# Performance work log

Hardware: AMD Instinct MI355X
Metric: run time of the kernel (lower is better)

The kernel has to match this reference:

```python
import jax, jax.numpy as jnp
import numpy as np

B, TZ, TU = 32, 16, 128
E, H, V = 512, 1024, 32000
FREQ_THRES = 4   # cfg.freq_thres: zero out copy prob for most-frequent tokens
LN_EPS = 1e-3


def setup_inputs() -> dict:
    key = jax.random.key(0)
    ks = jax.random.split(key, 16)
    s = lambda k, shape, sc=0.02: jax.random.normal(k, shape, jnp.float32) * sc
    return dict(
        z_enc_out=jax.random.normal(ks[0], (TZ, B, H), jnp.float32),
        pz_proba=jax.nn.softmax(jax.random.normal(ks[1], (TZ, B, V), jnp.float32), axis=-1),
        u_enc_out=jax.random.normal(ks[2], (TU, B, H), jnp.float32),
        m_t_input=jax.random.randint(ks[3], (1, B), 0, V),
        last_hidden=jax.random.normal(ks[4], (1, B, H), jnp.float32),
        emb=s(ks[5], (V, E), 1.0 / np.sqrt(E)),
        Wa_z=s(ks[6], (2 * H, H)), ba_z=jnp.zeros((H,), jnp.float32), v_z=s(ks[7], (H,), 1.0 / np.sqrt(H)),
        Wa_u=s(ks[8], (2 * H, H)), ba_u=jnp.zeros((H,), jnp.float32), v_u=s(ks[9], (H,), 1.0 / np.sqrt(H)),
        W_ih=s(ks[10], (3 * H, E + 2 * H)), W_hh=s(ks[11], (3 * H, H)),
        b_ih=jnp.zeros((3 * H,), jnp.float32), b_hh=jnp.zeros((3 * H,), jnp.float32),
        ln_a=jnp.ones((H,), jnp.float32), ln_b=jnp.zeros((H,), jnp.float32),
        W_proj=s(ks[12], (H, V)), b_proj=jnp.zeros((V,), jnp.float32),
        W_c=s(ks[13], (2 * H, H)), b_c=jnp.zeros((H,), jnp.float32),
        W_v1=s(ks[14], (H, 1)), b_v1=jnp.zeros((1,), jnp.float32),
    )


def _attn(hidden, enc, Wa, ba, v):
    # hidden [1,B,H], enc [T,B,H] -> context [1,B,H]
    hh = jnp.broadcast_to(hidden, enc.shape)                       # [T,B,H]
    energy = jnp.tanh(jnp.concatenate([hh, enc], -1) @ Wa + ba)    # [T,B,H]
    scores = jnp.einsum('tbh,h->bt', energy, v)                    # [B,T]
    w = jax.nn.softmax(scores, axis=1)
    return jnp.einsum('bt,tbh->bh', w, enc)[None]                  # [1,B,H]


def _layernorm(x, a, b):
    mu = jnp.mean(x, axis=-1, keepdims=True)
    sigma = jnp.std(x, axis=-1, keepdims=True, ddof=1)  # torch.std is unbiased
    return (x - mu) / (sigma + LN_EPS) * a + b


def reference(z_enc_out, pz_proba, u_enc_out, m_t_input, last_hidden,
              emb, Wa_z, ba_z, v_z, Wa_u, ba_u, v_u,
              W_ih, W_hh, b_ih, b_hh, ln_a, ln_b,
              W_proj, b_proj, W_c, b_c, W_v1, b_v1):
    m_embed = emb[m_t_input]                                       # [1,B,E]
    z_ctx = _attn(last_hidden, z_enc_out, Wa_z, ba_z, v_z)         # [1,B,H]
    u_ctx = _attn(last_hidden, u_enc_out, Wa_u, ba_u, v_u)         # [1,B,H]
    x = jnp.concatenate([z_ctx, u_ctx, m_embed], -1)[0]            # [B,2H+E]
    h = last_hidden[0]                                             # [B,H]
    # single-step GRU (torch gate order: r, z, n)
    gi = x @ W_ih.T + b_ih
    gh = h @ W_hh.T + b_hh
    ir, iz, inn = jnp.split(gi, 3, axis=-1)
    hr, hz, hn = jnp.split(gh, 3, axis=-1)
    r = jax.nn.sigmoid(ir + hr)
    zg = jax.nn.sigmoid(iz + hz)
    n = jnp.tanh(inn + r * hn)
    h_new = (1.0 - zg) * n + zg * h                                # [B,H]
    gru_out = _layernorm(h_new, ln_a, ln_b)                        # [B,H]
    gen_score = gru_out @ W_proj + b_proj                          # [B,V]
    # tanh-linear copy score over z positions
    g_rep = jnp.broadcast_to(gru_out[None], z_enc_out.shape)       # [Tz,B,H]
    zc = jnp.tanh(jnp.concatenate([z_enc_out, g_rep], -1) @ W_c + b_c)  # [Tz,B,H]
    zc = (zc @ W_v1 + b_v1)[..., 0].T                              # [B,Tz]
    # joint softmax over [gen | copy]
    scores = jax.nn.softmax(jnp.concatenate([gen_score, zc], axis=1), axis=1)
    gen_p, copy_p = scores[:, :V], scores[:, V:]
    copy_v = jnp.einsum('bt,tbv->bv', copy_p, pz_proba)            # mask_prob bmm
    freq_mask = (jnp.arange(V) >= FREQ_THRES).astype(gen_p.dtype)
    proba = gen_p + copy_v * freq_mask
    return proba, h_new[None]
```

## Files before the change

### kernel.cpp

```cpp
#include <hip/hip_runtime.h>
#include <stdint.h>

#define B_ 32
#define TZ_ 16
#define TU_ 128
#define E_ 512
#define H_ 1024
#define V_ 32000
#define X_ 2560
#define H3_ 3072
#define LN_EPS_ 0.001f

#define NP_IH 20
#define NP_HH 16

typedef unsigned short ushort_t;
typedef ushort_t us4 __attribute__((ext_vector_type(4)));
typedef ushort_t us8 __attribute__((ext_vector_type(8)));
typedef short bf16x8 __attribute__((ext_vector_type(8)));
typedef float f32x4 __attribute__((ext_vector_type(4)));

__device__ __forceinline__ float bf2f(ushort_t u){
  union { unsigned int i; float f; } x; x.i = ((unsigned int)u) << 16; return x.f;
}
__device__ __forceinline__ ushort_t f2b(float f){
  union { float f; unsigned int i; } u; u.f = f;
  unsigned int x = u.i;
  return (ushort_t)((x + 0x7fffu + ((x >> 16) & 1u)) >> 16);
}
__device__ __forceinline__ bool is_bf(const void* lnA){
  return *(const unsigned int*)lnA == 0x3F803F80u;
}
__device__ __forceinline__ float ldg_(const void* p, size_t i, bool isb){
  return isb ? bf2f(((const ushort_t*)p)[i]) : ((const float*)p)[i];
}
__device__ __forceinline__ float sigm(float x){ return 1.0f/(1.0f + __expf(-x)); }
__device__ __forceinline__ float tanh_f(float x){
  float cx = fminf(fmaxf(x, -9.0f), 9.0f);
  float t = __expf(2.0f*cx);
  return (t - 1.0f)/(t + 1.0f);
}

__global__ void k0_init(const void* lh, const void* emb, const int* mt,
                        const void* ba_z, const void* ba_u, const void* b_c, const void* bpj,
                        const void* lnA,
                        float* h_f32, ushort_t* hb, float* x, float* hWaZ, float* hWaU,
                        float* sz, float* su, float* gruWc, float* genscore){
  bool isb = is_bf(lnA);
  int i = blockIdx.x*256 + threadIdx.x;
  if (i < 32768){ float v = ldg_(lh, i, isb); h_f32[i] = v; hb[i] = f2b(v); return; }
  i -= 32768;
  if (i < 16384){ int b = i >> 9, e = i & 511;
    x[b*X_ + 2048 + e] = ldg_(emb, (size_t)(unsigned)mt[b]*E_ + e, isb); return; }
  i -= 16384;
  if (i < 32768){ hWaZ[i] = ldg_(ba_z, i & 1023, isb); return; }
  i -= 32768;
  if (i < 32768){ hWaU[i] = ldg_(ba_u, i & 1023, isb); return; }
  i -= 32768;
  if (i < 4608){ if (i < 512) sz[i] = 0.f; else su[i-512] = 0.f; return; }
  i -= 4608;
  if (i < 32768){ gruWc[i] = ldg_(b_c, i & 1023, isb); return; }
  i -= 32768;
  if (i < 1024000){
    int b = i / V_;
    int v = i - b*V_;
    genscore[(size_t)b*V_ + v] = ldg_(bpj, v, isb);
    return;
  }
}

__global__ void kC_cvt(const void* uenc, const void* zenc, const void* Wih, const void* Whh,
                       const void* lnA,
                       ushort_t* uB, ushort_t* zB, ushort_t* WihB, ushort_t* WhhB){
  bool isb = is_bf(lnA);
  long long i = (long long)(blockIdx.x*256 + threadIdx.x) * 8;
  const long long NU = (long long)TU_*B_*H_;
  const long long NZ = (long long)TZ_*B_*H_;
  const long long NI = (long long)H3_*X_;
  const long long NH = (long long)H3_*H_;
  const void* src; ushort_t* dst;
  if (i < NU){ src = uenc; dst = uB; }
  else if ((i -= NU) < NZ){ src = zenc; dst = zB; }
  else if ((i -= NZ) < NI){ src = Wih; dst = WihB; }
  else if ((i -= NI) < NH){ src = Whh; dst = WhhB; }
  else return;
  if (isb){
    *(us8*)&dst[i] = *(const us8*)((const ushort_t*)src + i);
  } else {
    const float* s = (const float*)src + i;
    float4 a0 = *(const float4*)s, a1 = *(const float4*)(s + 4);
    us8 o;
    o[0]=f2b(a0.x); o[1]=f2b(a0.y); o[2]=f2b(a0.z); o[3]=f2b(a0.w);
    o[4]=f2b(a1.x); o[5]=f2b(a1.y); o[6]=f2b(a1.z); o[7]=f2b(a1.w);
    *(us8*)&dst[i] = o;
  }
}

__global__ void kX_cvt(const float* x, ushort_t* xb){
  int i = (blockIdx.x*256 + threadIdx.x) * 8;
  const float* s = x + i;
  float4 a0 = *(const float4*)s, a1 = *(const float4*)(s + 4);
  us8 o;
  o[0]=f2b(a0.x); o[1]=f2b(a0.y); o[2]=f2b(a0.z); o[3]=f2b(a0.w);
  o[4]=f2b(a1.x); o[5]=f2b(a1.y); o[6]=f2b(a1.z); o[7]=f2b(a1.w);
  *(us8*)&xb[i] = o;
}

__global__ void kT_transpose(const void* Wz, const void* Wu, const void* Wc, const void* lnA,
                             ushort_t* tZ, ushort_t* tU, ushort_t* tC,
                             ushort_t* tZt, ushort_t* tUt, ushort_t* tCb){
  bool isb = is_bf(lnA);
  int w = blockIdx.z;
  const void* src = (w==0||w==3)? Wz : (w==1||w==4)? Wu : Wc;
  size_t base = (w==0||w==1||w==5) ? (size_t)H_*H_ : 0;
  ushort_t* dst = (w==0)? tZ : (w==1)? tU : (w==2)? tC : (w==3)? tZt : (w==4)? tUt : tCb;
  __shared__ ushort_t T[64][68];
  int k0 = blockIdx.x*64, j0 = blockIdx.y*64;
  int tx = threadIdx.x & 15, ty = threadIdx.x >> 4;
  if (isb){
    const ushort_t* s = (const ushort_t*)src + base;
    #pragma unroll
    for (int rr=0; rr<4; ++rr){
      int row = ty + rr*16;
      *(us4*)&T[row][tx*4] = *(const us4*)&s[(size_t)(k0+row)*H_ + j0 + tx*4];
    }
  } else {
    const float* s = (const float*)src + base;
    #pragma unroll
    for (int rr=0; rr<4; ++rr){
      int row = ty + rr*16;
      #pragma unroll
      for (int c=0;c<4;c++)
        T[row][tx*4+c] = f2b(s[(size_t)(k0+row)*H_ + j0 + tx*4 + c]);
    }
  }
  __syncthreads();
  #pragma unroll
  for (int rr=0; rr<4; ++rr){
    int row = ty + rr*16;
    us4 o;
    o[0]=T[tx*4+0][row]; o[1]=T[tx*4+1][row]; o[2]=T[tx*4+2][row]; o[3]=T[tx*4+3][row];
    *(us4*)&dst[(size_t)(j0+row)*H_ + k0 + tx*4] = o;
  }
}

__global__ void kP_t(const void* Wp, const void* lnA, ushort_t* WpT){
  bool isb = is_bf(lnA);
  __shared__ ushort_t T[64][68];
  int h0 = blockIdx.x*64, v0 = blockIdx.y*64;
  int tx = threadIdx.x & 15, ty = threadIdx.x >> 4;
  if (isb){
    const ushort_t* s = (const ushort_t*)Wp;
    #pragma unroll
    for (int rr=0; rr<4; ++rr){
      int row = ty + rr*16;
      *(us4*)&T[row][tx*4] = *(const us4*)&s[(size_t)(h0+row)*V_ + v0 + tx*4];
    }
  } else {
    const float* s = (const float*)Wp;
    #pragma unroll
    for (int rr=0; rr<4; ++rr){
      int row = ty + rr*16;
      #pragma unroll
      for (int c=0;c<4;c++)
        T[row][tx*4+c] = f2b(s[(size_t)(h0+row)*V_ + v0 + tx*4 + c]);
    }
  }
  __syncthreads();
  #pragma unroll
  for (int rr=0; rr<4; ++rr){
    int row = ty + rr*16;
    us4 o;
    o[0]=T[tx*4+0][row]; o[1]=T[tx*4+1][row]; o[2]=T[tx*4+2][row]; o[3]=T[tx*4+3][row];
    *(us4*)&WpT[(size_t)(v0+row)*H_ + h0 + tx*4] = o;
  }
}

__global__ __launch_bounds__(256) void kg_mfma(const ushort_t* Ab0, const ushort_t* Ab1,
                                               const ushort_t* W0, const ushort_t* W1,
                                               float* out0, float* out1, int N){
  const ushort_t* Ab = blockIdx.z ? Ab1 : Ab0;
  const ushort_t* WT = blockIdx.z ? W1 : W0;
  float* out = blockIdx.z ? out1 : out0;
  int j0 = blockIdx.x*128;
  int kchunk = H_ / gridDim.y;
  int kb = blockIdx.y*kchunk;
  __shared__ ushort_t Bs[128*32];
  int tid = threadIdx.x, wid = tid >> 6, lane = tid & 63;
  int q = lane >> 4, n = lane & 15;
  int rrow = tid >> 2, t4 = tid & 3;
  f32x4 acc[2][2];
  #pragma unroll
  for (int r=0;r<2;r++)
    #pragma unroll
    for (int c=0;c<2;c++)
      #pragma unroll
      for (int e=0;e<4;e++) acc[r][c][e] = 0.f;

  for (int kt = 0; kt < kchunk; kt += 32){
    int k = kb + kt;
    __syncthreads();
    #pragma unroll
    for (int p=0;p<2;p++){
      const ushort_t* srcB = WT + (size_t)(j0 + p*64 + rrow)*H_ + k + t4*8;
      __builtin_amdgcn_global_load_lds(srcB, &Bs[(p*64 + wid*16)*32], 16, 0, 0);
    }
    __syncthreads();
    bf16x8 af[2], bfr[2];
    #pragma unroll
    for (int r=0;r<2;r++) af[r] = *(const bf16x8*)&Ab[(size_t)(r*16 + n)*H_ + k + q*8];
    #pragma unroll
    for (int c=0;c<2;c++) bfr[c] = *(const bf16x8*)&Bs[(wid*32 + c*16 + n)*32 + q*8];
    #pragma unroll
    for (int r=0;r<2;r++)
      #pragma unroll
      for (int c=0;c<2;c++)
        acc[r][c] = __builtin_amdgcn_mfma_f32_16x16x32_bf16(af[r], bfr[c], acc[r][c], 0, 0, 0);
  }
  #pragma unroll
  for (int r=0;r<2;r++)
    #pragma unroll
    for (int c=0;c<2;c++)
      #pragma unroll
      for (int i=0;i<4;i++){
        int b = r*16 + q*4 + i;
        int j = j0 + wid*32 + c*16 + n;
        unsafeAtomicAdd(&out[(size_t)b*N + j], acc[r][c][i]);
      }
}

__global__ __launch_bounds__(256) void k2_mfma(const ushort_t* Ab, const ushort_t* WB,
                                               float* part, int K, int kchunk){
  int j0 = blockIdx.x*128;
  int kb = blockIdx.y*kchunk;
  __shared__ ushort_t Bs[128*32];
  int tid = threadIdx.x, wid = tid >> 6, lane = tid & 63;
  int q = lane >> 4, n = lane & 15;
  int rrow = tid >> 2, t4 = tid & 3;
  f32x4 acc[2][2];
  #pragma unroll
  for (int r=0;r<2;r++)
    #pragma unroll
    for (int c=0;c<2;c++)
      #pragma unroll
      for (int e=0;e<4;e++) acc[r][c][e] = 0.f;

  for (int kt = 0; kt < kchunk; kt += 32){
    int k = kb + kt;
    __syncthreads();
    #pragma unroll
    for (int p=0;p<2;p++){
      const ushort_t* srcB = WB + (size_t)(j0 + p*64 + rrow)*K + k + t4*8;
      __builtin_amdgcn_global_load_lds(srcB, &Bs[(p*64 + wid*16)*32], 16, 0, 0);
    }
    __syncthreads();
    bf16x8 af[2], bfr[2];
    #pragma unroll
    for (int r=0;r<2;r++) af[r] = *(const bf16x8*)&Ab[(size_t)(r*16 + n)*K + k + q*8];
    #pragma unroll
    for (int c=0;c<2;c++) bfr[c] = *(const bf16x8*)&Bs[(wid*32 + c*16 + n)*32 + q*8];
    #pragma unroll
    for (int r=0;r<2;r++)
      #pragma unroll
      for (int c=0;c<2;c++)
        acc[r][c] = __builtin_amdgcn_mfma_f32_16x16x32_bf16(af[r], bfr[c], acc[r][c], 0, 0, 0);
  }
  int p = blockIdx.y;
  #pragma unroll
  for (int r=0;r<2;r++)
    #pragma unroll
    for (int c=0;c<2;c++)
      #pragma unroll
      for (int i=0;i<4;i++){
        int b = r*16 + q*4 + i;
        int j = j0 + wid*32 + c*16 + n;
        part[(size_t)(p*32 + b)*H3_ + j] = acc[r][c][i];
      }
}

__global__ __launch_bounds__(256) void k3_mfma(
    const ushort_t* uB, const ushort_t* zB,
    const ushort_t* tU, const ushort_t* tZ, const ushort_t* tC,
    const float* hWaU, const float* hWaZ,
    const void* v_u, const void* v_z, const void* lnA,
    float* su, float* sz, float* zcpre)
{
  bool isb = is_bf(lnA);
  int which = blockIdx.z;
  int bx = blockIdx.x, nt = blockIdx.y;
  int mt;
  const ushort_t* A; const ushort_t* BT;
  if (which == 0){ A = uB; BT = tU; mt = bx; }
  else {
    int lo = (which==1) ? 8 : 12;
    if (bx < lo || bx >= lo+4) return;
    mt = bx - lo;
    A = zB; BT = (which==1) ? tZ : tC;
  }
  __shared__ ushort_t As[128*32];
  __shared__ ushort_t Bs[64*32];
  int tid = threadIdx.x;
  int wid = tid >> 6, lane = tid & 63;
  int q = lane >> 4, n = lane & 15;
  int wm = wid & 1, wn = wid >> 1;
  int r0 = mt*128, j0 = nt*64;
  f32x4 acc[4][2];
  #pragma unroll
  for (int a=0;a<4;a++)
    #pragma unroll
    for (int c=0;c<2;c++)
      #pragma unroll
      for (int e=0;e<4;e++) acc[a][c][e] = 0.f;

  int rrow = tid >> 2, t4 = tid & 3;

  for (int kt = 0; kt < 32; ++kt){
    __syncthreads();
    #pragma unroll
    for (int p=0;p<2;p++){
      const ushort_t* srcA = A + (size_t)(r0 + p*64 + rrow)*H_ + kt*32 + t4*8;
      __builtin_amdgcn_global_load_lds(srcA, &As[(p*64 + wid*16)*32], 16, 0, 0);
    }
    {
      const ushort_t* srcB = BT + (size_t)(j0 + rrow)*H_ + kt*32 + t4*8;
      __builtin_amdgcn_global_load_lds(srcB, &Bs[(wid*16)*32], 16, 0, 0);
    }
    __syncthreads();
    bf16x8 af[4], bfr[2];
    #pragma unroll
    for (int f=0;f<4;f++) af[f] = *(const bf16x8*)&As[(wm*64 + f*16 + n)*32 + q*8];
    #pragma unroll
    for (int f=0;f<2;f++) bfr[f] = *(const bf16x8*)&Bs[(wn*32 + f*16 + n)*32 + q*8];
    #pragma unroll
    for (int fr=0;fr<4;fr++)
      #pragma unroll
      for (int fn=0;fn<2;fn++)
        acc[fr][fn] = __builtin_amdgcn_mfma_f32_16x16x32_bf16(af[fr], bfr[fn], acc[fr][fn], 0, 0, 0);
  }

  if (which < 2){
    const float* pre = (which==0) ? hWaU : hWaZ;
    const void* vv = (which==0) ? v_u : v_z;
    float* score = (which==0) ? su : sz;
    float s[4][4];
    #pragma unroll
    for (int fr=0;fr<4;fr++)
      #pragma unroll
      for (int i=0;i<4;i++) s[fr][i]=0.f;
    #pragma unroll
    for (int fr=0;fr<4;fr++){
      #pragma unroll
      for (int fn=0;fn<2;fn++){
        int j  = j0 + wn*32 + fn*16 + n;
        float vj = ldg_(vv, j, isb);
        #pragma unroll
        for (int i=0;i<4;i++){
          int rl = wm*64 + fr*16 + q*4 + i;
          int b  = rl & 31;
          s[fr][i] += tanh_f(acc[fr][fn][i] + pre[b*H_ + j]) * vj;
        }
      }
    }
    #pragma unroll
    for (int fr=0;fr<4;fr++)
      #pragma unroll
      for (int i=0;i<4;i++){
        float t = s[fr][i];
        t += __shfl_xor(t, 1);
        t += __shfl_xor(t, 2);
        t += __shfl_xor(t, 4);
        t += __shfl_xor(t, 8);
        if (n == 0){
          int rl = wm*64 + fr*16 + q*4 + i;
          unsafeAtomicAdd(&score[r0 + rl], t);
        }
      }
  } else {
    #pragma unroll
    for (int fr=0;fr<4;fr++)
      #pragma unroll
      for (int fn=0;fn<2;fn++)
        #pragma unroll
        for (int i=0;i<4;i++){
          int rl = wm*64 + fr*16 + q*4 + i;
          int jl = wn*32 + fn*16 + n;
          zcpre[(size_t)(r0 + rl)*H_ + j0 + jl] = acc[fr][fn][i];
        }
  }
}

__global__ void k4_ctx(const float* sz, const float* su,
                       const void* zenc, const void* uenc, const void* lnA, float* x){
  bool isb = is_bf(lnA);
  int jc = blockIdx.x, b = blockIdx.y, which = blockIdx.z;
  int T = which ? TU_ : TZ_;
  const float* sc = which ? su : sz;
  const void* enc = which ? uenc : zenc;
  __shared__ float red[256];
  __shared__ float w[TU_];
  int tid = threadIdx.x;
  float v = (tid < T) ? sc[tid*B_ + b] : -1e30f;
  red[tid] = v; __syncthreads();
  for (int s=128; s>0; s>>=1){ if (tid < s) red[tid] = fmaxf(red[tid], red[tid+s]); __syncthreads(); }
  float m = red[0]; __syncthreads();
  float e = (tid < T) ? __expf(v - m) : 0.f;
  red[tid] = e; __syncthreads();
  for (int s=128; s>0; s>>=1){ if (tid < s) red[tid] += red[tid+s]; __syncthreads(); }
  float S = red[0]; __syncthreads();
  if (tid < T) w[tid] = e / S;
  __syncthreads();
  int j = jc*256 + tid;
  float acc = 0.f;
  #pragma unroll 4
  for (int t=0; t<T; ++t) acc = fmaf(w[t], ldg_(enc, (size_t)(t*B_ + b)*H_ + j, isb), acc);
  x[b*X_ + which*H_ + j] = acc;
}

__global__ __launch_bounds__(1024) void k5_gru(const float* gip, const float* ghp,
                       const void* b_ih, const void* b_hh,
                       const void* lh, const void* ln_a, const void* ln_b,
                       float* gru, ushort_t* grub, float* hout){
  bool isb = is_bf(ln_a);
  int b = blockIdx.x, tid = threadIdx.x;
  __shared__ float red[1024];
  int j = tid;
  float ir = ldg_(b_ih, j, isb), iz = ldg_(b_ih, 1024+j, isb), inn = ldg_(b_ih, 2048+j, isb);
  float hr = ldg_(b_hh, j, isb), hz = ldg_(b_hh, 1024+j, isb), hn = ldg_(b_hh, 2048+j, isb);
  #pragma unroll 4
  for (int p=0;p<NP_IH;p++){
    const float* gp = &gip[(size_t)(p*32 + b)*H3_];
    ir += gp[j]; iz += gp[1024+j]; inn += gp[2048+j];
  }
  #pragma unroll 4
  for (int p=0;p<NP_HH;p++){
    const float* gp = &ghp[(size_t)(p*32 + b)*H3_];
    hr += gp[j]; hz += gp[1024+j]; hn += gp[2048+j];
  }
  float hv = ldg_(lh, b*H_ + j, isb);
  float r  = sigm(ir + hr);
  float zg = sigm(iz + hz);
  float nn = tanh_f(inn + r*hn);
  float h2 = (1.f - zg)*nn + zg*hv;
  hout[b*H_ + j] = h2;
  red[tid] = h2; __syncthreads();
  for (int s=512;s>0;s>>=1){ if(tid<s) red[tid]+=red[tid+s]; __syncthreads(); }
  float mu = red[0] / 1024.f; __syncthreads();
  red[tid] = h2*h2; __syncthreads();
  for (int s=512;s>0;s>>=1){ if(tid<s) red[tid]+=red[tid+s]; __syncthreads(); }
  float var = (red[0] - 1024.f*mu*mu) / 1023.f;
  float sg = sqrtf(fmaxf(var, 0.f));
  float inv = 1.f/(sg + LN_EPS_);
  float g = (h2 - mu)*inv*ldg_(ln_a, j, isb) + ldg_(ln_b, j, isb);
  gru[b*H_ + j] = g;
  grub[b*H_ + j] = f2b(g);
}

__global__ void k7_zc(const float* zcpre, const float* gruWc, const void* Wv1,
                      const void* b_v1, const void* lnA, float* zc){
  bool isb = is_bf(lnA);
  int r = blockIdx.x, b = r & 31, tid = threadIdx.x;
  __shared__ float red[256];
  float s = 0.f;
  #pragma unroll
  for (int jj=0;jj<4;jj++){
    int j = tid + jj*256;
    float e = tanh_f(zcpre[(size_t)r*H_ + j] + gruWc[b*H_ + j]);
    s = fmaf(e, ldg_(Wv1, j, isb), s);
  }
  red[tid] = s; __syncthreads();
  for (int st=128;st>0;st>>=1){ if(tid<st) red[tid]+=red[tid+st]; __syncthreads(); }
  if (tid==0) zc[r] = red[0] + ldg_(b_v1, 0, isb);
}

__global__ void k8a(const float* genscore, float* statpart){
  int v = blockIdx.x*256 + threadIdx.x;
  int b = blockIdx.y, tid = threadIdx.x;
  __shared__ float red[256];
  float g = genscore[(size_t)b*V_ + v];
  red[tid] = g; __syncthreads();
  for (int s=128;s>0;s>>=1){ if(tid<s) red[tid]=fmaxf(red[tid],red[tid+s]); __syncthreads(); }
  float m = red[0]; __syncthreads();
  float e = __expf(g - m);
  red[tid] = e; __syncthreads();
  for (int s=128;s>0;s>>=1){ if(tid<s) red[tid]+=red[tid+s]; __syncthreads(); }
  if (tid==0){ statpart[(b*125 + blockIdx.x)*2] = m; statpart[(b*125 + blockIdx.x)*2+1] = red[0]; }
}

__global__ void k8b(const float* statpart, const float* zc, float* stats, float* copyp){
  int b = blockIdx.x, tid = threadIdx.x;
  __shared__ float red[128];
  float m = -1e30f, s = 0.f;
  if (tid < 125){ m = statpart[(b*125 + tid)*2]; s = statpart[(b*125 + tid)*2 + 1]; }
  float zv = (tid < 16) ? zc[tid*B_ + b] : -1e30f;
  red[tid] = fmaxf(m, zv); __syncthreads();
  for (int st=64;st>0;st>>=1){ if(tid<st) red[tid]=fmaxf(red[tid],red[tid+st]); __syncthreads(); }
  float M = red[0]; __syncthreads();
  float zp = (tid < 125) ? s*__expf(m - M) : 0.f;
  if (tid < 16) zp += __expf(zv - M);
  red[tid] = zp; __syncthreads();
  for (int st=64;st>0;st>>=1){ if(tid<st) red[tid]+=red[tid+st]; __syncthreads(); }
  float invZ = 1.f/red[0];
  if (tid < 16) copyp[b*16 + tid] = __expf(zv - M)*invZ;
  if (tid == 0){ stats[b*2] = M; stats[b*2+1] = invZ; }
}

__global__ void k8c(const float* genscore, const float* stats, const float* copyp,
                    const void* pz, const void* lnA, float* out){
  bool isb = is_bf(lnA);
  int v = blockIdx.x*256 + threadIdx.x;
  int b = blockIdx.y;
  float M = stats[b*2], invZ = stats[b*2+1];
  float p = __expf(genscore[(size_t)b*V_ + v] - M)*invZ;
  if (v >= 4){
    float cv = 0.f;
    if (isb){
      const ushort_t* pzp = (const ushort_t*)pz;
      #pragma unroll
      for (int t=0;t<16;t++)
        cv = fmaf(copyp[b*16 + t], bf2f(pzp[(size_t)(t*B_ + b)*V_ + v]), cv);
    } else {
      const float* pzp = (const float*)pz;
      #pragma unroll
      for (int t=0;t<16;t++)
        cv = fmaf(copyp[b*16 + t], pzp[(size_t)(t*B_ + b)*V_ + v], cv);
    }
    p += cv;
  }
  out[(size_t)b*V_ + v] = p;
}

extern "C" void kernel_launch(void* const* d_in, const int* in_sizes, int n_in,
                              void* d_out, int out_size, void* d_ws, size_t ws_size,
                              hipStream_t stream){
  const void* z_enc = d_in[0];
  const void* pz    = d_in[1];
  const void* u_enc = d_in[2];
  const int*  m_t   = (const int*)d_in[3];
  const void* lh    = d_in[4];
  const void* emb   = d_in[5];
  const void* Wa_z  = d_in[6];
  const void* ba_z  = d_in[7];
  const void* v_z   = d_in[8];
  const void* Wa_u  = d_in[9];
  const void* ba_u  = d_in[10];
  const void* v_u   = d_in[11];
  const void* W_ih  = d_in[12];
  const void* W_hh  = d_in[13];
  const void* b_ih  = d_in[14];
  const void* b_hh  = d_in[15];
  const void* ln_a  = d_in[16];
  const void* ln_b  = d_in[17];
  const void* W_proj= d_in[18];
  const void* b_proj= d_in[19];
  const void* W_c   = d_in[20];
  const void* b_c   = d_in[21];
  const void* W_v1  = d_in[22];
  const void* b_v1  = d_in[23];

  float* wsf = (float*)d_ws;
  size_t o = 0;
  auto alloc = [&](size_t n){ float* p = wsf + o; o += n; return p; };
  float* h_f32 = alloc(B_*H_);
  float* x     = alloc(B_*X_);
  float* hWaZ  = alloc(B_*H_);
  float* hWaU  = alloc(B_*H_);
  float* sz    = alloc(TZ_*B_);
  float* su    = alloc(TU_*B_);
  float* gru   = alloc(B_*H_);
  float* gruWc = alloc(B_*H_);
  float* zcpre = alloc((size_t)TZ_*B_*H_);
  float* zcv   = alloc(TZ_*B_);
  float* ghp   = alloc((size_t)NP_HH*B_*H3_);
  float* gip   = alloc((size_t)NP_IH*B_*H3_);
  float* genscore = alloc((size_t)B_*V_);
  float* statpart = alloc(B_*125*2);
  float* stats = alloc(B_*2);
  float* copyp = alloc(B_*TZ_);
  o = (o + 7) & ~(size_t)7;
  ushort_t* wT = (ushort_t*)(wsf + o);
  ushort_t* tZ  = wT;
  ushort_t* tU  = wT + (size_t)H_*H_;
  ushort_t* tC  = wT + (size_t)2*H_*H_;
  ushort_t* tZt = wT + (size_t)3*H_*H_;
  ushort_t* tUt = wT + (size_t)4*H_*H_;
  ushort_t* tCb = wT + (size_t)5*H_*H_;
  o += (size_t)6*H_*H_/2;
  ushort_t* uB = (ushort_t*)(wsf + o);
  o += (size_t)TU_*B_*H_/2;
  ushort_t* zB = (ushort_t*)(wsf + o);
  o += (size_t)TZ_*B_*H_/2;
  ushort_t* WihB = (ushort_t*)(wsf + o);
  o += (size_t)H3_*X_/2;
  ushort_t* WhhB = (ushort_t*)(wsf + o);
  o += (size_t)H3_*H_/2;
  ushort_t* xb = (ushort_t*)(wsf + o);
  o += (size_t)B_*X_/2;
  ushort_t* hb = (ushort_t*)(wsf + o);
  o += (size_t)B_*H_/2;
  ushort_t* grub = (ushort_t*)(wsf + o);
  o += (size_t)B_*H_/2;
  ushort_t* WpT = (ushort_t*)(wsf + o);
  o += (size_t)V_*H_/2;
  float* outp = (float*)d_out;
  float* hout = outp + (size_t)B_*V_;

  k0_init<<<4594, 256, 0, stream>>>(lh, emb, m_t, ba_z, ba_u, b_c, b_proj, ln_a,
                                    h_f32, hb, x, hWaZ, hWaU, sz, su, gruWc, genscore);
  kC_cvt<<<7680, 256, 0, stream>>>(u_enc, z_enc, W_ih, W_hh, ln_a, uB, zB, WihB, WhhB);
  kP_t<<<dim3(16,500), 256, 0, stream>>>(W_proj, ln_a, WpT);
  kT_transpose<<<dim3(16,16,6), 256, 0, stream>>>(Wa_z, Wa_u, W_c, ln_a, tZ, tU, tC, tZt, tUt, tCb);
  kg_mfma<<<dim3(8,8,2), 256, 0, stream>>>(hb, hb, tZt, tUt, hWaZ, hWaU, H_);
  k2_mfma<<<dim3(24,NP_HH), 256, 0, stream>>>(hb, WhhB, ghp, H_, 64);
  k3_mfma<<<dim3(32,16,3), 256, 0, stream>>>(uB, zB, tU, tZ, tC, hWaU, hWaZ, v_u, v_z, ln_a, su, sz, zcpre);
  k4_ctx<<<dim3(4,32,2), 256, 0, stream>>>(sz, su, z_enc, u_enc, ln_a, x);
  kX_cvt<<<40, 256, 0, stream>>>(x, xb);
  k2_mfma<<<dim3(24,NP_IH), 256, 0, stream>>>(xb, WihB, gip, X_, 128);
  k5_gru<<<32, 1024, 0, stream>>>(gip, ghp, b_ih, b_hh, lh, ln_a, ln_b, gru, grub, hout);
  kg_mfma<<<dim3(8,8,1), 256, 0, stream>>>(grub, grub, tCb, tCb, gruWc, gruWc, H_);
  k7_zc<<<512, 256, 0, stream>>>(zcpre, gruWc, W_v1, b_v1, ln_a, zcv);
  kg_mfma<<<dim3(250,4,1), 256, 0, stream>>>(grub, grub, WpT, WpT, genscore, genscore, V_);
  k8a<<<dim3(125,32), 256, 0, stream>>>(genscore, statpart);
  k8b<<<32, 128, 0, stream>>>(statpart, zcv, stats, copyp);
  k8c<<<dim3(125,32), 256, 0, stream>>>(genscore, stats, copyp, pz, ln_a, outp);
}
```

Measured before the change: 512.6 us.

## Read W_proj directly in projection GEMM and atomically reduce split-K GRU partials

Result: faster. 460.9 us (-10.1%).

```diff
diff --git a/kernel.cpp b/kernel.cpp
--- a/kernel.cpp
+++ b/kernel.cpp
@@ -11,9 +11,6 @@
 #define H3_ 3072
 #define LN_EPS_ 0.001f
 
-#define NP_IH 20
-#define NP_HH 16
-
 typedef unsigned short ushort_t;
 typedef ushort_t us4 __attribute__((ext_vector_type(4)));
 typedef ushort_t us8 __attribute__((ext_vector_type(8)));
@@ -42,16 +39,18 @@
 }
 
 __global__ void k0_init(const void* lh, const void* emb, const int* mt,
-                        const void* ba_z, const void* ba_u, const void* b_c, const void* bpj,
+                        const void* ba_z, const void* ba_u, const void* b_c,
+                        const void* b_ih, const void* b_hh, const void* bpj,
                         const void* lnA,
-                        float* h_f32, ushort_t* hb, float* x, float* hWaZ, float* hWaU,
-                        float* sz, float* su, float* gruWc, float* genscore){
+                        ushort_t* hb, ushort_t* xb, float* hWaZ, float* hWaU,
+                        float* sz, float* su, float* gruWc, float* gi, float* gh,
+                        float* genscore){
   bool isb = is_bf(lnA);
   int i = blockIdx.x*256 + threadIdx.x;
-  if (i < 32768){ float v = ldg_(lh, i, isb); h_f32[i] = v; hb[i] = f2b(v); return; }
+  if (i < 32768){ hb[i] = f2b(ldg_(lh, i, isb)); return; }
   i -= 32768;
   if (i < 16384){ int b = i >> 9, e = i & 511;
-    x[b*X_ + 2048 + e] = ldg_(emb, (size_t)(unsigned)mt[b]*E_ + e, isb); return; }
+    xb[b*X_ + 2048 + e] = f2b(ldg_(emb, (size_t)(unsigned)mt[b]*E_ + e, isb)); return; }
   i -= 16384;
   if (i < 32768){ hWaZ[i] = ldg_(ba_z, i & 1023, isb); return; }
   i -= 32768;
@@ -61,11 +60,14 @@
   i -= 4608;
   if (i < 32768){ gruWc[i] = ldg_(b_c, i & 1023, isb); return; }
   i -= 32768;
+  if (i < 98304){ gi[i] = ldg_(b_ih, i % H3_, isb); return; }
+  i -= 98304;
+  if (i < 98304){ gh[i] = ldg_(b_hh, i % H3_, isb); return; }
+  i -= 98304;
   if (i < 1024000){
     int b = i / V_;
     int v = i - b*V_;
     genscore[(size_t)b*V_ + v] = ldg_(bpj, v, isb);
-    return;
   }
 }
 
@@ -96,16 +98,6 @@
   }
 }
 
-__global__ void kX_cvt(const float* x, ushort_t* xb){
-  int i = (blockIdx.x*256 + threadIdx.x) * 8;
-  const float* s = x + i;
-  float4 a0 = *(const float4*)s, a1 = *(const float4*)(s + 4);
-  us8 o;
-  o[0]=f2b(a0.x); o[1]=f2b(a0.y); o[2]=f2b(a0.z); o[3]=f2b(a0.w);
-  o[4]=f2b(a1.x); o[5]=f2b(a1.y); o[6]=f2b(a1.z); o[7]=f2b(a1.w);
-  *(us8*)&xb[i] = o;
-}
-
 __global__ void kT_transpose(const void* Wz, const void* Wu, const void* Wc, const void* lnA,
                              ushort_t* tZ, ushort_t* tU, ushort_t* tC,
                              ushort_t* tZt, ushort_t* tUt, ushort_t* tCb){
@@ -141,38 +133,6 @@
     us4 o;
     o[0]=T[tx*4+0][row]; o[1]=T[tx*4+1][row]; o[2]=T[tx*4+2][row]; o[3]=T[tx*4+3][row];
     *(us4*)&dst[(size_t)(j0+row)*H_ + k0 + tx*4] = o;
-  }
-}
-
-__global__ void kP_t(const void* Wp, const void* lnA, ushort_t* WpT){
-  bool isb = is_bf(lnA);
-  __shared__ ushort_t T[64][68];
-  int h0 = blockIdx.x*64, v0 = blockIdx.y*64;
-  int tx = threadIdx.x & 15, ty = threadIdx.x >> 4;
-  if (isb){
-    const ushort_t* s = (const ushort_t*)Wp;
-    #pragma unroll
-    for (int rr=0; rr<4; ++rr){
-      int row = ty + rr*16;
-      *(us4*)&T[row][tx*4] = *(const us4*)&s[(size_t)(h0+row)*V_ + v0 + tx*4];
-    }
-  } else {
-    const float* s = (const float*)Wp;
-    #pragma unroll
-    for (int rr=0; rr<4; ++rr){
-      int row = ty + rr*16;
-      #pragma unroll
-      for (int c=0;c<4;c++)
-        T[row][tx*4+c] = f2b(s[(size_t)(h0+row)*V_ + v0 + tx*4 + c]);
-    }
-  }
-  __syncthreads();
-  #pragma unroll
-  for (int rr=0; rr<4; ++rr){
-    int row = ty + rr*16;
-    us4 o;
-    o[0]=T[tx*4+0][row]; o[1]=T[tx*4+1][row]; o[2]=T[tx*4+2][row]; o[3]=T[tx*4+3][row];
-    *(us4*)&WpT[(size_t)(v0+row)*H_ + h0 + tx*4] = o;
   }
 }
 
@@ -230,7 +190,7 @@
 }
 
 __global__ __launch_bounds__(256) void k2_mfma(const ushort_t* Ab, const ushort_t* WB,
-                                               float* part, int K, int kchunk){
+                                               float* out, int K, int kchunk){
   int j0 = blockIdx.x*128;
   int kb = blockIdx.y*kchunk;
   __shared__ ushort_t Bs[128*32];
@@ -265,7 +225,6 @@
       for (int c=0;c<2;c++)
         acc[r][c] = __builtin_amdgcn_mfma_f32_16x16x32_bf16(af[r], bfr[c], acc[r][c], 0, 0, 0);
   }
-  int p = blockIdx.y;
   #pragma unroll
   for (int r=0;r<2;r++)
     #pragma unroll
@@ -274,7 +233,72 @@
       for (int i=0;i<4;i++){
         int b = r*16 + q*4 + i;
         int j = j0 + wid*32 + c*16 + n;
-        part[(size_t)(p*32 + b)*H3_ + j] = acc[r][c][i];
+        unsafeAtomicAdd(&out[(size_t)b*H3_ + j], acc[r][c][i]);
+      }
+}
+
+__global__ __launch_bounds__(256) void k6p_mfma(const ushort_t* grub, const void* Wp,
+                                                const void* lnA, float* genscore){
+  bool isb = is_bf(lnA);
+  int j0 = blockIdx.x*128;
+  int kb = blockIdx.y*256;
+  __shared__ float Ts[32][129];
+  int tid = threadIdx.x, wid = tid >> 6, lane = tid & 63;
+  int q = lane >> 4, n = lane & 15;
+  int lrow = tid >> 3, lcol = (tid & 7)*16;
+  f32x4 acc[2][2];
+  #pragma unroll
+  for (int r=0;r<2;r++)
+    #pragma unroll
+    for (int c=0;c<2;c++)
+      #pragma unroll
+      for (int e=0;e<4;e++) acc[r][c][e] = 0.f;
+
+  for (int kt = 0; kt < 256; kt += 32){
+    int k = kb + kt;
+    __syncthreads();
+    if (isb){
+      const ushort_t* s = (const ushort_t*)Wp + (size_t)(k + lrow)*V_ + j0 + lcol;
+      us8 a0 = *(const us8*)s;
+      us8 a1 = *(const us8*)(s + 8);
+      #pragma unroll
+      for (int e=0;e<8;e++){ Ts[lrow][lcol+e] = bf2f(a0[e]); Ts[lrow][lcol+8+e] = bf2f(a1[e]); }
+    } else {
+      const float* s = (const float*)Wp + (size_t)(k + lrow)*V_ + j0 + lcol;
+      float4 f0 = *(const float4*)s,     f1 = *(const float4*)(s+4);
+      float4 f2 = *(const float4*)(s+8), f3 = *(const float4*)(s+12);
+      *(float4*)&Ts[lrow][lcol]    = f0;
+      *(float4*)&Ts[lrow][lcol+4]  = f1;
+      *(float4*)&Ts[lrow][lcol+8]  = f2;
+      *(float4*)&Ts[lrow][lcol+12] = f3;
+    }
+    __syncthreads();
+    bf16x8 af[2], bfr[2];
+    #pragma unroll
+    for (int r=0;r<2;r++) af[r] = *(const bf16x8*)&grub[(size_t)(r*16 + n)*H_ + k + q*8];
+    #pragma unroll
+    for (int c=0;c<2;c++){
+      int vl = wid*32 + c*16 + n;
+      us8 o;
+      #pragma unroll
+      for (int e=0;e<8;e++) o[e] = f2b(Ts[q*8 + e][vl]);
+      bfr[c] = *(bf16x8*)&o;
+    }
+    #pragma unroll
+    for (int r=0;r<2;r++)
+      #pragma unroll
+      for (int c=0;c<2;c++)
+        acc[r][c] = __builtin_amdgcn_mfma_f32_16x16x32_bf16(af[r], bfr[c], acc[r][c], 0, 0, 0);
+  }
+  #pragma unroll
+  for (int r=0;r<2;r++)
+    #pragma unroll
+    for (int c=0;c<2;c++)
+      #pragma unroll
+      for (int i=0;i<4;i++){
+        int b = r*16 + q*4 + i;
+        int v = j0 + wid*32 + c*16 + n;
+        unsafeAtomicAdd(&genscore[(size_t)b*V_ + v], acc[r][c][i]);
       }
 }
 
@@ -390,7 +414,7 @@
 }
 
 __global__ void k4_ctx(const float* sz, const float* su,
-                       const void* zenc, const void* uenc, const void* lnA, float* x){
+                       const void* zenc, const void* uenc, const void* lnA, ushort_t* xb){
   bool isb = is_bf(lnA);
   int jc = blockIdx.x, b = blockIdx.y, which = blockIdx.z;
   int T = which ? TU_ : TZ_;
@@ -413,29 +437,18 @@
   float acc = 0.f;
   #pragma unroll 4
   for (int t=0; t<T; ++t) acc = fmaf(w[t], ldg_(enc, (size_t)(t*B_ + b)*H_ + j, isb), acc);
-  x[b*X_ + which*H_ + j] = acc;
-}
-
-__global__ __launch_bounds__(1024) void k5_gru(const float* gip, const float* ghp,
-                       const void* b_ih, const void* b_hh,
+  xb[b*X_ + which*H_ + j] = f2b(acc);
+}
+
+__global__ __launch_bounds__(1024) void k5_gru(const float* gi, const float* gh,
                        const void* lh, const void* ln_a, const void* ln_b,
-                       float* gru, ushort_t* grub, float* hout){
+                       ushort_t* grub, float* hout){
   bool isb = is_bf(ln_a);
   int b = blockIdx.x, tid = threadIdx.x;
   __shared__ float red[1024];
   int j = tid;
-  float ir = ldg_(b_ih, j, isb), iz = ldg_(b_ih, 1024+j, isb), inn = ldg_(b_ih, 2048+j, isb);
-  float hr = ldg_(b_hh, j, isb), hz = ldg_(b_hh, 1024+j, isb), hn = ldg_(b_hh, 2048+j, isb);
-  #pragma unroll 4
-  for (int p=0;p<NP_IH;p++){
-    const float* gp = &gip[(size_t)(p*32 + b)*H3_];
-    ir += gp[j]; iz += gp[1024+j]; inn += gp[2048+j];
-  }
-  #pragma unroll 4
-  for (int p=0;p<NP_HH;p++){
-    const float* gp = &ghp[(size_t)(p*32 + b)*H3_];
-    hr += gp[j]; hz += gp[1024+j]; hn += gp[2048+j];
-  }
+  float ir = gi[(size_t)b*H3_ + j], iz = gi[(size_t)b*H3_ + 1024 + j], inn = gi[(size_t)b*H3_ + 2048 + j];
+  float hr = gh[(size_t)b*H3_ + j], hz = gh[(size_t)b*H3_ + 1024 + j], hn = gh[(size_t)b*H3_ + 2048 + j];
   float hv = ldg_(lh, b*H_ + j, isb);
   float r  = sigm(ir + hr);
   float zg = sigm(iz + hz);
@@ -451,7 +464,6 @@
   float sg = sqrtf(fmaxf(var, 0.f));
   float inv = 1.f/(sg + LN_EPS_);
   float g = (h2 - mu)*inv*ldg_(ln_a, j, isb) + ldg_(ln_b, j, isb);
-  gru[b*H_ + j] = g;
   grub[b*H_ + j] = f2b(g);
 }
 
@@ -560,18 +572,15 @@
   float* wsf = (float*)d_ws;
   size_t o = 0;
   auto alloc = [&](size_t n){ float* p = wsf + o; o += n; return p; };
-  float* h_f32 = alloc(B_*H_);
-  float* x     = alloc(B_*X_);
   float* hWaZ  = alloc(B_*H_);
   float* hWaU  = alloc(B_*H_);
   float* sz    = alloc(TZ_*B_);
   float* su    = alloc(TU_*B_);
-  float* gru   = alloc(B_*H_);
   float* gruWc = alloc(B_*H_);
   float* zcpre = alloc((size_t)TZ_*B_*H_);
   float* zcv   = alloc(TZ_*B_);
-  float* ghp   = alloc((size_t)NP_HH*B_*H3_);
-  float* gip   = alloc((size_t)NP_IH*B_*H3_);
+  float* gi    = alloc((size_t)B_*H3_);
+  float* gh    = alloc((size_t)B_*H3_);
   float* genscore = alloc((size_t)B_*V_);
   float* statpart = alloc(B_*125*2);
   float* stats = alloc(B_*2);
@@ -599,26 +608,22 @@
   o += (size_t)B_*H_/2;
   ushort_t* grub = (ushort_t*)(wsf + o);
   o += (size_t)B_*H_/2;
-  ushort_t* WpT = (ushort_t*)(wsf + o);
-  o += (size_t)V_*H_/2;
   float* outp = (float*)d_out;
   float* hout = outp + (size_t)B_*V_;
 
-  k0_init<<<4594, 256, 0, stream>>>(lh, emb, m_t, ba_z, ba_u, b_c, b_proj, ln_a,
-                                    h_f32, hb, x, hWaZ, hWaU, sz, su, gruWc, genscore);
+  k0_init<<<5362, 256, 0, stream>>>(lh, emb, m_t, ba_z, ba_u, b_c, b_ih, b_hh, b_proj, ln_a,
+                                    hb, xb, hWaZ, hWaU, sz, su, gruWc, gi, gh, genscore);
   kC_cvt<<<7680, 256, 0, stream>>>(u_enc, z_enc, W_ih, W_hh, ln_a, uB, zB, WihB, WhhB);
-  kP_t<<<dim3(16,500), 256, 0, stream>>>(W_proj, ln_a, WpT);
   kT_transpose<<<dim3(16,16,6), 256, 0, stream>>>(Wa_z, Wa_u, W_c, ln_a, tZ, tU, tC, tZt, tUt, tCb);
   kg_mfma<<<dim3(8,8,2), 256, 0, stream>>>(hb, hb, tZt, tUt, hWaZ, hWaU, H_);
-  k2_mfma<<<dim3(24,NP_HH), 256, 0, stream>>>(hb, WhhB, ghp, H_, 64);
+  k2_mfma<<<dim3(24,16), 256, 0, stream>>>(hb, WhhB, gh, H_, 64);
   k3_mfma<<<dim3(32,16,3), 256, 0, stream>>>(uB, zB, tU, tZ, tC, hWaU, hWaZ, v_u, v_z, ln_a, su, sz, zcpre);
-  k4_ctx<<<dim3(4,32,2), 256, 0, stream>>>(sz, su, z_enc, u_enc, ln_a, x);
-  kX_cvt<<<40, 256, 0, stream>>>(x, xb);
-  k2_mfma<<<dim3(24,NP_IH), 256, 0, stream>>>(xb, WihB, gip, X_, 128);
-  k5_gru<<<32, 1024, 0, stream>>>(gip, ghp, b_ih, b_hh, lh, ln_a, ln_b, gru, grub, hout);
+  k4_ctx<<<dim3(4,32,2), 256, 0, stream>>>(sz, su, z_enc, u_enc, ln_a, xb);
+  k2_mfma<<<dim3(24,20), 256, 0, stream>>>(xb, WihB, gi, X_, 128);
+  k5_gru<<<32, 1024, 0, stream>>>(gi, gh, lh, ln_a, ln_b, grub, hout);
   kg_mfma<<<dim3(8,8,1), 256, 0, stream>>>(grub, grub, tCb, tCb, gruWc, gruWc, H_);
   k7_zc<<<512, 256, 0, stream>>>(zcpre, gruWc, W_v1, b_v1, ln_a, zcv);
-  kg_mfma<<<dim3(250,4,1), 256, 0, stream>>>(grub, grub, WpT, WpT, genscore, genscore, V_);
+  k6p_mfma<<<dim3(250,4), 256, 0, stream>>>(grub, W_proj, ln_a, genscore);
   k8a<<<dim3(125,32), 256, 0, stream>>>(genscore, statpart);
   k8b<<<32, 128, 0, stream>>>(statpart, zcv, stats, copyp);
   k8c<<<dim3(125,32), 256, 0, stream>>>(genscore, stats, copyp, pz, ln_a, outp);
```
